# Kernel tuning notes

Measured on AMD Instinct MI355X. Metric: run time of the kernel, lower is better.

## Reference

```python
import jax, jax.numpy as jnp
import numpy as np

B, N, XDIM, EDIM, H = 4, 256, 256, 128, 8
DF = XDIM // H


def _linear_params(key, din, dout):
    k1, k2 = jax.random.split(key)
    s = 1.0 / np.sqrt(din)
    W = jax.random.uniform(k1, (din, dout), minval=-s, maxval=s, dtype=jnp.float32)
    b = jax.random.uniform(k2, (dout,), minval=-s, maxval=s, dtype=jnp.float32)
    return W, b


def setup_inputs() -> dict:
    key = jax.random.key(0)
    ks = jax.random.split(key, 9)
    x = jax.random.normal(ks[0], (B, N, XDIM), dtype=jnp.float32)
    e = jax.random.normal(ks[1], (B, N, N, EDIM), dtype=jnp.float32)
    Wq, bq = _linear_params(ks[2], XDIM, XDIM)
    Wk, bk = _linear_params(ks[3], XDIM, XDIM)
    Wv, bv = _linear_params(ks[4], XDIM, XDIM)
    Wem, bem = _linear_params(ks[5], EDIM, XDIM)  # e_mul
    Wea, bea = _linear_params(ks[6], EDIM, XDIM)  # e_add
    Wxo, bxo = _linear_params(ks[7], XDIM, XDIM)  # x_out
    Weo, beo = _linear_params(ks[8], XDIM, EDIM)  # e_out
    return {"x": x, "e": e, "Wq": Wq, "bq": bq, "Wk": Wk, "bk": bk,
            "Wv": Wv, "bv": bv, "Wem": Wem, "bem": bem, "Wea": Wea, "bea": bea,
            "Wxo": Wxo, "bxo": bxo, "Weo": Weo, "beo": beo}


def reference(x, e, Wq, bq, Wk, bk, Wv, bv, Wem, bem, Wea, bea, Wxo, bxo, Weo, beo):
    Bq, Nq, _ = x.shape
    # per-node projections -> [B, N, H, DF]
    Q = (x @ Wq + bq).reshape(Bq, Nq, H, DF)
    K = (x @ Wk + bk).reshape(Bq, Nq, H, DF)
    V = (x @ Wv + bv).reshape(Bq, Nq, H, DF)
    # broadcasted outer product: Y[b,i,j,h,d] = Q[b,i,h,d] * K[b,j,h,d] / sqrt(DF)
    Y = Q[:, :, None] * K[:, None] * (1.0 / np.sqrt(DF))  # [B,N,N,H,DF]
    # edge modulation
    E1 = (e @ Wem + bem).reshape(Bq, Nq, Nq, H, DF)
    E2 = (e @ Wea + bea).reshape(Bq, Nq, Nq, H, DF)
    Y = Y * (E1 + 1.0) + E2
    # new edge features
    newE = Y.reshape(Bq, Nq, Nq, XDIM) @ Weo + beo  # [B,N,N,EDIM]
    # attention: softmax over the FIRST node axis (dim=1), as in the torch code
    attn = jax.nn.softmax(Y, axis=1)  # [B,N,N,H,DF]
    # weighted_V[b,j,h,d] = sum_i attn[b,i,j,h,d] * V[b,j,h,d]
    weighted_V = jnp.sum(attn * V[:, None], axis=1)  # [B,N,H,DF]
    newX = weighted_V.reshape(Bq, Nq, XDIM) @ Wxo + bxo  # [B,N,XDIM]
    return (newX, newE)
```

## Files before the change

kernel.cpp:

```cpp
#include <hip/hip_runtime.h>

#define NN 256
#define XD 256
#define ED 128

typedef __attribute__((ext_vector_type(8))) short short8;
typedef __attribute__((ext_vector_type(4))) float f32x4;
typedef __attribute__((ext_vector_type(2))) unsigned int uint2v;

__device__ __forceinline__ unsigned short f2bf(float f) {
    unsigned u = __builtin_bit_cast(unsigned, f);
    u += 0x7FFF + ((u >> 16) & 1);
    return (unsigned short)(u >> 16);
}

__device__ __forceinline__ unsigned cvtpk(float lo, float hi) {
    unsigned r;
    asm("v_cvt_pk_bf16_f32 %0, %1, %2" : "=v"(r) : "v"(lo), "v"(hi));
    return r;
}

#define MFMA16(a, b, c) __builtin_amdgcn_mfma_f32_16x16x32_bf16(a, b, c, 0, 0, 0)

__global__ __launch_bounds__(256) void wprep_kernel(
    const float* __restrict__ Wq, const float* __restrict__ Wk,
    const float* __restrict__ Wv, const float* __restrict__ Wxo,
    const float* __restrict__ Wem, const float* __restrict__ Wea,
    const float* __restrict__ Weo,
    short* __restrict__ WqT, short* __restrict__ WkT,
    short* __restrict__ WvT, short* __restrict__ WxoT,
    short* __restrict__ WemT, short* __restrict__ WeaT,
    short* __restrict__ WeoT)
{
    __shared__ float sT[32][33];
    int blk = blockIdx.x;
    const float* src; short* dst; int din, dout, tile;
    if (blk < 256) {
        int m = blk >> 6; tile = blk & 63; din = 256; dout = 256;
        src = m == 0 ? Wq : (m == 1 ? Wk : (m == 2 ? Wv : Wxo));
        dst = m == 0 ? WqT : (m == 1 ? WkT : (m == 2 ? WvT : WxoT));
    } else if (blk < 320) {
        int m = (blk - 256) >> 5; tile = (blk - 256) & 31; din = 128; dout = 256;
        src = m == 0 ? Wem : Wea; dst = m == 0 ? WemT : WeaT;
    } else {
        tile = blk - 320; din = 256; dout = 128;
        src = Weo; dst = WeoT;
    }
    int ksh = (din == 256) ? 3 : 2;
    int kt = tile & ((1 << ksh) - 1);
    int nt = tile >> ksh;
    int c = threadIdx.x & 31, rbase = threadIdx.x >> 5;
    #pragma unroll
    for (int p = 0; p < 4; ++p) {
        int r = rbase + p * 8;
        sT[r][c] = src[(kt * 32 + r) * dout + nt * 32 + c];
    }
    __syncthreads();
    #pragma unroll
    for (int p = 0; p < 4; ++p) {
        int r = rbase + p * 8;
        dst[(nt * 32 + r) * din + kt * 32 + c] = (short)f2bf(sT[c][r]);
    }
}

__global__ __launch_bounds__(512) void proj_all_kernel(
    const float* __restrict__ x,
    const short* __restrict__ WqT, const short* __restrict__ WkT,
    const short* __restrict__ WvT, const short* __restrict__ WxoT,
    const float* __restrict__ bq, const float* __restrict__ bk,
    const float* __restrict__ bv, const float* __restrict__ bxo,
    float* __restrict__ Qs, float* __restrict__ Ks, float* __restrict__ outX)
{
    __shared__ unsigned short sX[64 * 264];
    __shared__ unsigned short sV[64 * 264];
    const int blk = blockIdx.x;
    const bool isvx = blk >= 32;
    const int mtile = isvx ? (blk - 32) : (blk >> 1);
    const int tid = threadIdx.x, wave = tid >> 6, lane = tid & 63;
    const int quad = lane >> 4, l16 = lane & 15;

    {
        const float4* src4 = (const float4*)(x + (size_t)mtile * 64 * XD);
        #pragma unroll
        for (int it = 0; it < 8; ++it) {
            int idx4 = tid + it * 512;
            float4 v = src4[idx4];
            int elem = idx4 * 4, row = elem >> 8, col = elem & 255;
            uint2v p; p.x = cvtpk(v.x, v.y); p.y = cvtpk(v.z, v.w);
            *(uint2v*)&sX[row * 264 + col] = p;
        }
    }
    __syncthreads();

    const int c0 = wave * 32;

    if (!isvx) {
        const int mat  = blk & 1;
        const short* WT   = mat ? WkT : WqT;
        const float* bias = mat ? bk : bq;
        const float scale = mat ? 1.0f : 0.17677669529663687f;
        float* out        = mat ? Ks : Qs;
        f32x4 acc[4][2] = {};
        for (int ks = 0; ks < 8; ++ks) {
            short8 bfrag[2];
            #pragma unroll
            for (int ct = 0; ct < 2; ++ct)
                bfrag[ct] = *(const short8*)&WT[(c0 + ct * 16 + l16) * 256 + ks * 32 + quad * 8];
            #pragma unroll
            for (int mt = 0; mt < 4; ++mt) {
                short8 a = *(const short8*)&sX[(mt * 16 + l16) * 264 + ks * 32 + quad * 8];
                acc[mt][0] = MFMA16(a, bfrag[0], acc[mt][0]);
                acc[mt][1] = MFMA16(a, bfrag[1], acc[mt][1]);
            }
        }
        #pragma unroll
        for (int mt = 0; mt < 4; ++mt)
            #pragma unroll
            for (int ct = 0; ct < 2; ++ct) {
                int cc = c0 + ct * 16 + l16;
                float bb = bias[cc];
                #pragma unroll
                for (int r = 0; r < 4; ++r)
                    out[(size_t)(mtile * 64 + mt * 16 + quad * 4 + r) * 256 + cc] =
                        (acc[mt][ct][r] + bb) * scale;
            }
    } else {
        f32x4 acc[4][2] = {};
        for (int ks = 0; ks < 8; ++ks) {
            short8 bfrag[2];
            #pragma unroll
            for (int ct = 0; ct < 2; ++ct)
                bfrag[ct] = *(const short8*)&WvT[(c0 + ct * 16 + l16) * 256 + ks * 32 + quad * 8];
            #pragma unroll
            for (int mt = 0; mt < 4; ++mt) {
                short8 a = *(const short8*)&sX[(mt * 16 + l16) * 264 + ks * 32 + quad * 8];
                acc[mt][0] = MFMA16(a, bfrag[0], acc[mt][0]);
                acc[mt][1] = MFMA16(a, bfrag[1], acc[mt][1]);
            }
        }
        #pragma unroll
        for (int mt = 0; mt < 4; ++mt)
            #pragma unroll
            for (int ct = 0; ct < 2; ++ct) {
                int cc = c0 + ct * 16 + l16;
                float bb = bv[cc];
                #pragma unroll
                for (int r = 0; r < 4; ++r)
                    sV[(mt * 16 + quad * 4 + r) * 264 + cc] = f2bf(acc[mt][ct][r] + bb);
            }
        __syncthreads();
        f32x4 acc2[4][2] = {};
        for (int ks = 0; ks < 8; ++ks) {
            short8 bfrag[2];
            #pragma unroll
            for (int ct = 0; ct < 2; ++ct)
                bfrag[ct] = *(const short8*)&WxoT[(c0 + ct * 16 + l16) * 256 + ks * 32 + quad * 8];
            #pragma unroll
            for (int mt = 0; mt < 4; ++mt) {
                short8 a = *(const short8*)&sV[(mt * 16 + l16) * 264 + ks * 32 + quad * 8];
                acc2[mt][0] = MFMA16(a, bfrag[0], acc2[mt][0]);
                acc2[mt][1] = MFMA16(a, bfrag[1], acc2[mt][1]);
            }
        }
        #pragma unroll
        for (int mt = 0; mt < 4; ++mt)
            #pragma unroll
            for (int ct = 0; ct < 2; ++ct) {
                int cc = c0 + ct * 16 + l16;
                float bb = bxo[cc];
                #pragma unroll
                for (int r = 0; r < 4; ++r)
                    outX[(size_t)(mtile * 64 + mt * 16 + quad * 4 + r) * 256 + cc] =
                        acc2[mt][ct][r] + bb;
            }
    }
}

__global__ __launch_bounds__(256, 3) void fused_edge_kernel(
    const float* __restrict__ e, const float* __restrict__ Qs,
    const float* __restrict__ Ks, const short* __restrict__ WemT,
    const short* __restrict__ WeaT, const short* __restrict__ WeoT,
    const float* __restrict__ bem, const float* __restrict__ bea,
    const float* __restrict__ beo, float* __restrict__ outE)
{
    __shared__ unsigned short sE[64 * 140];
    __shared__ unsigned short sY[64 * 268];

    const int blk  = blockIdx.x;
    const int jq   = blk & 3;
    const int i    = (blk >> 2) & 255;
    const int b    = blk >> 10;
    const int j0   = jq * 64;
    const int tid  = threadIdx.x;
    const int wave = tid >> 6;
    const int lane = tid & 63;
    const int quad = lane >> 4;
    const int l16  = lane & 15;

    {
        const float4* src4 = (const float4*)(e + (size_t)((b * NN + i) * NN + j0) * ED);
        float4 ev[8];
        #pragma unroll
        for (int it = 0; it < 8; ++it) ev[it] = src4[tid + it * 256];
        #pragma unroll
        for (int it = 0; it < 8; ++it) {
            int idx4 = tid + it * 256;
            int row = idx4 >> 5, col = (idx4 & 31) * 4;
            uint2v p; p.x = cvtpk(ev[it].x, ev[it].y); p.y = cvtpk(ev[it].z, ev[it].w);
            *(uint2v*)&sE[row * 140 + col] = p;
        }
    }
    __syncthreads();

    const int cW = wave * 64;
    const float* Qrow = Qs + (size_t)(b * NN + i) * XD;

    short8 ef[4][4];
    #pragma unroll
    for (int jT = 0; jT < 4; ++jT)
        #pragma unroll
        for (int ks = 0; ks < 4; ++ks)
            ef[jT][ks] = *(const short8*)&sE[(jT * 16 + l16) * 140 + ks * 32 + quad * 8];

    #pragma unroll
    for (int cT = 0; cT < 4; ++cT) {
        const int c0 = cW + cT * 16;
        const int cq = c0 + quad * 4;
        f32x4 q4  = *(const f32x4*)&Qrow[cq];
        f32x4 bm4 = *(const f32x4*)&bem[cq] + 1.0f;
        f32x4 ba4 = *(const f32x4*)&bea[cq];
        f32x4 k4[4];
        #pragma unroll
        for (int jT = 0; jT < 4; ++jT)
            k4[jT] = *(const f32x4*)&Ks[(size_t)(b * NN + j0 + jT * 16 + l16) * XD + cq];

        f32x4 a1[4] = {}, a2[4] = {};
        #pragma unroll
        for (int ks = 0; ks < 4; ++ks) {
            short8 wa = *(const short8*)&WemT[(c0 + l16) * 128 + ks * 32 + quad * 8];
            short8 wb = *(const short8*)&WeaT[(c0 + l16) * 128 + ks * 32 + quad * 8];
            #pragma unroll
            for (int jT = 0; jT < 4; ++jT) {
                a1[jT] = MFMA16(wa, ef[jT][ks], a1[jT]);
                a2[jT] = MFMA16(wb, ef[jT][ks], a2[jT]);
            }
        }
        #pragma unroll
        for (int jT = 0; jT < 4; ++jT) {
            f32x4 y = q4 * k4[jT] * (a1[jT] + bm4) + (a2[jT] + ba4);
            uint2v p; p.x = cvtpk(y[0], y[1]); p.y = cvtpk(y[2], y[3]);
            *(uint2v*)&sY[(jT * 16 + l16) * 268 + cq] = p;
        }
    }

    const int oW = wave * 32;
    short8 wo[4][2];
    #pragma unroll
    for (int ks = 0; ks < 4; ++ks)
        #pragma unroll
        for (int oT = 0; oT < 2; ++oT)
            wo[ks][oT] = *(const short8*)&WeoT[(oW + oT * 16 + l16) * 256 + ks * 32 + quad * 8];
    __syncthreads();

    f32x4 acc[2][4] = {};
    #pragma unroll
    for (int ks = 0; ks < 8; ++ks) {
        short8 w0, w1;
        if (ks < 4) { w0 = wo[ks][0]; w1 = wo[ks][1]; }
        else {
            w0 = *(const short8*)&WeoT[(oW + l16) * 256 + ks * 32 + quad * 8];
            w1 = *(const short8*)&WeoT[(oW + 16 + l16) * 256 + ks * 32 + quad * 8];
        }
        #pragma unroll
        for (int jT = 0; jT < 4; ++jT) {
            short8 yb = *(const short8*)&sY[(jT * 16 + l16) * 268 + ks * 32 + quad * 8];
            acc[0][jT] = MFMA16(w0, yb, acc[0][jT]);
            acc[1][jT] = MFMA16(w1, yb, acc[1][jT]);
        }
    }

    float* outBase = outE + (size_t)((b * NN + i) * NN + j0) * ED;
    #pragma unroll
    for (int oT = 0; oT < 2; ++oT) {
        const int oq = oW + oT * 16 + quad * 4;
        f32x4 bo4 = *(const f32x4*)&beo[oq];
        #pragma unroll
        for (int jT = 0; jT < 4; ++jT) {
            f32x4 st = acc[oT][jT] + bo4;
            *(f32x4*)&outBase[(size_t)(j0 * 0 + jT * 16 + l16) * ED + oq] = st;
        }
    }
}

extern "C" void kernel_launch(void* const* d_in, const int* in_sizes, int n_in,
                              void* d_out, int out_size, void* d_ws, size_t ws_size,
                              hipStream_t stream)
{
    const float* x   = (const float*)d_in[0];
    const float* e   = (const float*)d_in[1];
    const float* Wq  = (const float*)d_in[2];
    const float* bq  = (const float*)d_in[3];
    const float* Wk  = (const float*)d_in[4];
    const float* bk  = (const float*)d_in[5];
    const float* Wv  = (const float*)d_in[6];
    const float* bv  = (const float*)d_in[7];
    const float* Wem = (const float*)d_in[8];
    const float* bem = (const float*)d_in[9];
    const float* Wea = (const float*)d_in[10];
    const float* bea = (const float*)d_in[11];
    const float* Wxo = (const float*)d_in[12];
    const float* bxo = (const float*)d_in[13];
    const float* Weo = (const float*)d_in[14];
    const float* beo = (const float*)d_in[15];

    float* outX = (float*)d_out;
    float* outE = (float*)d_out + 262144;

    float* Qs   = (float*)d_ws;
    float* Ks   = Qs + 262144;
    short* WqT  = (short*)(Ks + 262144);
    short* WkT  = WqT + 65536;
    short* WvT  = WkT + 65536;
    short* WxoT = WvT + 65536;
    short* WemT = WxoT + 65536;
    short* WeaT = WemT + 32768;
    short* WeoT = WeaT + 32768;

    hipLaunchKernelGGL(wprep_kernel, dim3(352), dim3(256), 0, stream,
                       Wq, Wk, Wv, Wxo, Wem, Wea, Weo,
                       WqT, WkT, WvT, WxoT, WemT, WeaT, WeoT);
    hipLaunchKernelGGL(proj_all_kernel, dim3(48), dim3(512), 0, stream,
                       x, WqT, WkT, WvT, WxoT, bq, bk, bv, bxo, Qs, Ks, outX);
    hipLaunchKernelGGL(fused_edge_kernel, dim3(4096), dim3(256), 0, stream,
                       e, Qs, Ks, WemT, WeaT, WeoT, bem, bea, beo, outE);
}
```

Before: 381.4 us.

## Loop each edge block over four j-tiles with register-prefetched next e tile

The edge kernel now launches one block per (b,i) row and loops over the four 64-column j tiles, instead of one block per tile. While the Weo GEMM runs, the next e tile is loaded into registers and written to shared memory afterwards, so global latency overlaps with MFMA work. The output GEMM is also remapped so each wave covers 64 output columns × 2 j-tiles, which changes how Weo fragments and Y are reused. The cost is a quarter as many blocks (1024 on a large GPU), more live registers, and extra barriers per iteration.

```diff
diff --git a/kernel.cpp b/kernel.cpp
--- a/kernel.cpp
+++ b/kernel.cpp
@@ -187,21 +187,20 @@
     __shared__ unsigned short sY[64 * 268];
 
     const int blk  = blockIdx.x;
-    const int jq   = blk & 3;
-    const int i    = (blk >> 2) & 255;
-    const int b    = blk >> 10;
-    const int j0   = jq * 64;
+    const int i    = blk & 255;
+    const int b    = blk >> 8;
     const int tid  = threadIdx.x;
     const int wave = tid >> 6;
     const int lane = tid & 63;
     const int quad = lane >> 4;
     const int l16  = lane & 15;
 
+    const float4* ebase = (const float4*)(e + (size_t)((b * NN + i) * NN) * ED);
+
     {
-        const float4* src4 = (const float4*)(e + (size_t)((b * NN + i) * NN + j0) * ED);
         float4 ev[8];
         #pragma unroll
-        for (int it = 0; it < 8; ++it) ev[it] = src4[tid + it * 256];
+        for (int it = 0; it < 8; ++it) ev[it] = ebase[tid + it * 256];
         #pragma unroll
         for (int it = 0; it < 8; ++it) {
             int idx4 = tid + it * 256;
@@ -212,83 +211,99 @@
     }
     __syncthreads();
 
+    const float* Qrow = Qs + (size_t)(b * NN + i) * XD;
     const int cW = wave * 64;
-    const float* Qrow = Qs + (size_t)(b * NN + i) * XD;
-
-    short8 ef[4][4];
-    #pragma unroll
-    for (int jT = 0; jT < 4; ++jT)
-        #pragma unroll
-        for (int ks = 0; ks < 4; ++ks)
-            ef[jT][ks] = *(const short8*)&sE[(jT * 16 + l16) * 140 + ks * 32 + quad * 8];
-
-    #pragma unroll
-    for (int cT = 0; cT < 4; ++cT) {
-        const int c0 = cW + cT * 16;
-        const int cq = c0 + quad * 4;
-        f32x4 q4  = *(const f32x4*)&Qrow[cq];
-        f32x4 bm4 = *(const f32x4*)&bem[cq] + 1.0f;
-        f32x4 ba4 = *(const f32x4*)&bea[cq];
-        f32x4 k4[4];
+    const int oH = (wave & 1) * 64;
+    const int jH = (wave >> 1) * 2;
+
+    #pragma unroll 1
+    for (int t = 0; t < 4; ++t) {
+        const int j0 = t * 64;
+
+        short8 efr[4][4];
         #pragma unroll
         for (int jT = 0; jT < 4; ++jT)
-            k4[jT] = *(const f32x4*)&Ks[(size_t)(b * NN + j0 + jT * 16 + l16) * XD + cq];
-
-        f32x4 a1[4] = {}, a2[4] = {};
-        #pragma unroll
-        for (int ks = 0; ks < 4; ++ks) {
-            short8 wa = *(const short8*)&WemT[(c0 + l16) * 128 + ks * 32 + quad * 8];
-            short8 wb = *(const short8*)&WeaT[(c0 + l16) * 128 + ks * 32 + quad * 8];
+            #pragma unroll
+            for (int ks = 0; ks < 4; ++ks)
+                efr[jT][ks] = *(const short8*)&sE[(jT * 16 + l16) * 140 + ks * 32 + quad * 8];
+
+        #pragma unroll
+        for (int cT = 0; cT < 4; ++cT) {
+            const int c0 = cW + cT * 16;
+            const int cq = c0 + quad * 4;
+            f32x4 q4  = *(const f32x4*)&Qrow[cq];
+            f32x4 bm4 = *(const f32x4*)&bem[cq] + 1.0f;
+            f32x4 ba4 = *(const f32x4*)&bea[cq];
+            f32x4 k4[4];
+            #pragma unroll
+            for (int jT = 0; jT < 4; ++jT)
+                k4[jT] = *(const f32x4*)&Ks[(size_t)(b * NN + j0 + jT * 16 + l16) * XD + cq];
+
+            f32x4 a1[4] = {}, a2[4] = {};
+            #pragma unroll
+            for (int ks = 0; ks < 4; ++ks) {
+                short8 wa = *(const short8*)&WemT[(c0 + l16) * 128 + ks * 32 + quad * 8];
+                short8 wb = *(const short8*)&WeaT[(c0 + l16) * 128 + ks * 32 + quad * 8];
+                #pragma unroll
+                for (int jT = 0; jT < 4; ++jT) {
+                    a1[jT] = MFMA16(wa, efr[jT][ks], a1[jT]);
+                    a2[jT] = MFMA16(wb, efr[jT][ks], a2[jT]);
+                }
+            }
             #pragma unroll
             for (int jT = 0; jT < 4; ++jT) {
-                a1[jT] = MFMA16(wa, ef[jT][ks], a1[jT]);
-                a2[jT] = MFMA16(wb, ef[jT][ks], a2[jT]);
-            }
-        }
-        #pragma unroll
-        for (int jT = 0; jT < 4; ++jT) {
-            f32x4 y = q4 * k4[jT] * (a1[jT] + bm4) + (a2[jT] + ba4);
-            uint2v p; p.x = cvtpk(y[0], y[1]); p.y = cvtpk(y[2], y[3]);
-            *(uint2v*)&sY[(jT * 16 + l16) * 268 + cq] = p;
-        }
-    }
-
-    const int oW = wave * 32;
-    short8 wo[4][2];
-    #pragma unroll
-    for (int ks = 0; ks < 4; ++ks)
-        #pragma unroll
-        for (int oT = 0; oT < 2; ++oT)
-            wo[ks][oT] = *(const short8*)&WeoT[(oW + oT * 16 + l16) * 256 + ks * 32 + quad * 8];
-    __syncthreads();
-
-    f32x4 acc[2][4] = {};
-    #pragma unroll
-    for (int ks = 0; ks < 8; ++ks) {
-        short8 w0, w1;
-        if (ks < 4) { w0 = wo[ks][0]; w1 = wo[ks][1]; }
-        else {
-            w0 = *(const short8*)&WeoT[(oW + l16) * 256 + ks * 32 + quad * 8];
-            w1 = *(const short8*)&WeoT[(oW + 16 + l16) * 256 + ks * 32 + quad * 8];
-        }
-        #pragma unroll
-        for (int jT = 0; jT < 4; ++jT) {
-            short8 yb = *(const short8*)&sY[(jT * 16 + l16) * 268 + ks * 32 + quad * 8];
-            acc[0][jT] = MFMA16(w0, yb, acc[0][jT]);
-            acc[1][jT] = MFMA16(w1, yb, acc[1][jT]);
-        }
-    }
-
-    float* outBase = outE + (size_t)((b * NN + i) * NN + j0) * ED;
-    #pragma unroll
-    for (int oT = 0; oT < 2; ++oT) {
-        const int oq = oW + oT * 16 + quad * 4;
-        f32x4 bo4 = *(const f32x4*)&beo[oq];
-        #pragma unroll
-        for (int jT = 0; jT < 4; ++jT) {
-            f32x4 st = acc[oT][jT] + bo4;
-            *(f32x4*)&outBase[(size_t)(j0 * 0 + jT * 16 + l16) * ED + oq] = st;
-        }
+                f32x4 y = q4 * k4[jT] * (a1[jT] + bm4) + (a2[jT] + ba4);
+                uint2v p; p.x = cvtpk(y[0], y[1]); p.y = cvtpk(y[2], y[3]);
+                *(uint2v*)&sY[(jT * 16 + l16) * 268 + cq] = p;
+            }
+        }
+        __syncthreads();
+
+        float4 ev[8];
+        if (t < 3) {
+            #pragma unroll
+            for (int it = 0; it < 8; ++it)
+                ev[it] = ebase[(t + 1) * 2048 + tid + it * 256];
+        }
+
+        f32x4 acc[4][2] = {};
+        #pragma unroll
+        for (int ks = 0; ks < 8; ++ks) {
+            short8 wo[4];
+            #pragma unroll
+            for (int oT = 0; oT < 4; ++oT)
+                wo[oT] = *(const short8*)&WeoT[(oH + oT * 16 + l16) * 256 + ks * 32 + quad * 8];
+            #pragma unroll
+            for (int jt = 0; jt < 2; ++jt) {
+                short8 yb = *(const short8*)&sY[((jH + jt) * 16 + l16) * 268 + ks * 32 + quad * 8];
+                #pragma unroll
+                for (int oT = 0; oT < 4; ++oT)
+                    acc[oT][jt] = MFMA16(wo[oT], yb, acc[oT][jt]);
+            }
+        }
+
+        if (t < 3) {
+            #pragma unroll
+            for (int it = 0; it < 8; ++it) {
+                int idx4 = tid + it * 256;
+                int row = idx4 >> 5, col = (idx4 & 31) * 4;
+                uint2v p; p.x = cvtpk(ev[it].x, ev[it].y); p.y = cvtpk(ev[it].z, ev[it].w);
+                *(uint2v*)&sE[row * 140 + col] = p;
+            }
+        }
+
+        float* outBase = outE + (size_t)((b * NN + i) * NN + j0) * ED;
+        #pragma unroll
+        for (int oT = 0; oT < 4; ++oT) {
+            const int oq = oH + oT * 16 + quad * 4;
+            f32x4 bo4 = *(const f32x4*)&beo[oq];
+            #pragma unroll
+            for (int jt = 0; jt < 2; ++jt) {
+                f32x4 st = acc[oT][jt] + bo4;
+                *(f32x4*)&outBase[(size_t)((jH + jt) * 16 + l16) * ED + oq] = st;
+            }
+        }
+        __syncthreads();
     }
 }
 
@@ -331,6 +346,6 @@
                        WqT, WkT, WvT, WxoT, WemT, WeaT, WeoT);
     hipLaunchKernelGGL(proj_all_kernel, dim3(48), dim3(512), 0, stream,
                        x, WqT, WkT, WvT, WxoT, bq, bk, bv, bxo, Qs, Ks, outX);
-    hipLaunchKernelGGL(fused_edge_kernel, dim3(4096), dim3(256), 0, stream,
+    hipLaunchKernelGGL(fused_edge_kernel, dim3(1024), dim3(256), 0, stream,
                        e, Qs, Ks, WemT, WeaT, WeoT, bem, bea, beo, outE);
 }
```

After: 553.0 us. +45.0%, slower.

## Split edge kernel Y computation into two halves to shrink LDS and raise occupancy

Applied to the files above, without the earlier changes.

The fused edge kernel now computes the 256-wide Y tile in two 128-column passes, each followed by its half of the e_out GEMM reduction. This halves the sY shared buffer, and the e fragments are re-read from LDS instead of being held in registers, so launch bounds can request 4 blocks per SM instead of 3. The cost is extra barriers, repeated LDS reads of the e tile, and weight fragments that are no longer preloaded.

```diff
diff --git a/kernel.cpp b/kernel.cpp
--- a/kernel.cpp
+++ b/kernel.cpp
@@ -176,7 +176,7 @@
     }
 }
 
-__global__ __launch_bounds__(256, 3) void fused_edge_kernel(
+__global__ __launch_bounds__(256, 4) void fused_edge_kernel(
     const float* __restrict__ e, const float* __restrict__ Qs,
     const float* __restrict__ Ks, const short* __restrict__ WemT,
     const short* __restrict__ WeaT, const short* __restrict__ WeoT,
@@ -184,7 +184,7 @@
     const float* __restrict__ beo, float* __restrict__ outE)
 {
     __shared__ unsigned short sE[64 * 140];
-    __shared__ unsigned short sY[64 * 268];
+    __shared__ unsigned short sY[64 * 140];
 
     const int blk  = blockIdx.x;
     const int jq   = blk & 3;
@@ -212,71 +212,58 @@
     }
     __syncthreads();
 
-    const int cW = wave * 64;
     const float* Qrow = Qs + (size_t)(b * NN + i) * XD;
-
-    short8 ef[4][4];
+    const int oW = wave * 32;
+    f32x4 acc[2][4] = {};
+
     #pragma unroll
-    for (int jT = 0; jT < 4; ++jT)
-        #pragma unroll
-        for (int ks = 0; ks < 4; ++ks)
-            ef[jT][ks] = *(const short8*)&sE[(jT * 16 + l16) * 140 + ks * 32 + quad * 8];
-
-    #pragma unroll
-    for (int cT = 0; cT < 4; ++cT) {
-        const int c0 = cW + cT * 16;
-        const int cq = c0 + quad * 4;
-        f32x4 q4  = *(const f32x4*)&Qrow[cq];
-        f32x4 bm4 = *(const f32x4*)&bem[cq] + 1.0f;
-        f32x4 ba4 = *(const f32x4*)&bea[cq];
-        f32x4 k4[4];
-        #pragma unroll
-        for (int jT = 0; jT < 4; ++jT)
-            k4[jT] = *(const f32x4*)&Ks[(size_t)(b * NN + j0 + jT * 16 + l16) * XD + cq];
-
-        f32x4 a1[4] = {}, a2[4] = {};
+    for (int p = 0; p < 2; ++p) {
+        #pragma unroll
+        for (int cT = 0; cT < 2; ++cT) {
+            const int cl = wave * 32 + cT * 16;
+            const int c0 = p * 128 + cl;
+            const int cq = c0 + quad * 4;
+            f32x4 q4  = *(const f32x4*)&Qrow[cq];
+            f32x4 bm4 = *(const f32x4*)&bem[cq] + 1.0f;
+            f32x4 ba4 = *(const f32x4*)&bea[cq];
+            f32x4 k4[4];
+            #pragma unroll
+            for (int jT = 0; jT < 4; ++jT)
+                k4[jT] = *(const f32x4*)&Ks[(size_t)(b * NN + j0 + jT * 16 + l16) * XD + cq];
+
+            f32x4 a1[4] = {}, a2[4] = {};
+            #pragma unroll
+            for (int ks = 0; ks < 4; ++ks) {
+                short8 wa = *(const short8*)&WemT[(c0 + l16) * 128 + ks * 32 + quad * 8];
+                short8 wb = *(const short8*)&WeaT[(c0 + l16) * 128 + ks * 32 + quad * 8];
+                #pragma unroll
+                for (int jT = 0; jT < 4; ++jT) {
+                    short8 ef = *(const short8*)&sE[(jT * 16 + l16) * 140 + ks * 32 + quad * 8];
+                    a1[jT] = MFMA16(wa, ef, a1[jT]);
+                    a2[jT] = MFMA16(wb, ef, a2[jT]);
+                }
+            }
+            #pragma unroll
+            for (int jT = 0; jT < 4; ++jT) {
+                f32x4 y = q4 * k4[jT] * (a1[jT] + bm4) + (a2[jT] + ba4);
+                uint2v pk; pk.x = cvtpk(y[0], y[1]); pk.y = cvtpk(y[2], y[3]);
+                *(uint2v*)&sY[(jT * 16 + l16) * 140 + cl + quad * 4] = pk;
+            }
+        }
+        __syncthreads();
+
         #pragma unroll
         for (int ks = 0; ks < 4; ++ks) {
-            short8 wa = *(const short8*)&WemT[(c0 + l16) * 128 + ks * 32 + quad * 8];
-            short8 wb = *(const short8*)&WeaT[(c0 + l16) * 128 + ks * 32 + quad * 8];
+            short8 w0 = *(const short8*)&WeoT[(oW + l16) * 256 + (p * 4 + ks) * 32 + quad * 8];
+            short8 w1 = *(const short8*)&WeoT[(oW + 16 + l16) * 256 + (p * 4 + ks) * 32 + quad * 8];
             #pragma unroll
             for (int jT = 0; jT < 4; ++jT) {
-                a1[jT] = MFMA16(wa, ef[jT][ks], a1[jT]);
-                a2[jT] = MFMA16(wb, ef[jT][ks], a2[jT]);
-            }
-        }
-        #pragma unroll
-        for (int jT = 0; jT < 4; ++jT) {
-            f32x4 y = q4 * k4[jT] * (a1[jT] + bm4) + (a2[jT] + ba4);
-            uint2v p; p.x = cvtpk(y[0], y[1]); p.y = cvtpk(y[2], y[3]);
-            *(uint2v*)&sY[(jT * 16 + l16) * 268 + cq] = p;
-        }
-    }
-
-    const int oW = wave * 32;
-    short8 wo[4][2];
-    #pragma unroll
-    for (int ks = 0; ks < 4; ++ks)
-        #pragma unroll
-        for (int oT = 0; oT < 2; ++oT)
-            wo[ks][oT] = *(const short8*)&WeoT[(oW + oT * 16 + l16) * 256 + ks * 32 + quad * 8];
-    __syncthreads();
-
-    f32x4 acc[2][4] = {};
-    #pragma unroll
-    for (int ks = 0; ks < 8; ++ks) {
-        short8 w0, w1;
-        if (ks < 4) { w0 = wo[ks][0]; w1 = wo[ks][1]; }
-        else {
-            w0 = *(const short8*)&WeoT[(oW + l16) * 256 + ks * 32 + quad * 8];
-            w1 = *(const short8*)&WeoT[(oW + 16 + l16) * 256 + ks * 32 + quad * 8];
-        }
-        #pragma unroll
-        for (int jT = 0; jT < 4; ++jT) {
-            short8 yb = *(const short8*)&sY[(jT * 16 + l16) * 268 + ks * 32 + quad * 8];
-            acc[0][jT] = MFMA16(w0, yb, acc[0][jT]);
-            acc[1][jT] = MFMA16(w1, yb, acc[1][jT]);
-        }
+                short8 yb = *(const short8*)&sY[(jT * 16 + l16) * 140 + ks * 32 + quad * 8];
+                acc[0][jT] = MFMA16(w0, yb, acc[0][jT]);
+                acc[1][jT] = MFMA16(w1, yb, acc[1][jT]);
+            }
+        }
+        if (p == 0) __syncthreads();
     }
 
     float* outBase = outE + (size_t)((b * NN + i) * NN + j0) * ED;
@@ -287,7 +274,7 @@
         #pragma unroll
         for (int jT = 0; jT < 4; ++jT) {
             f32x4 st = acc[oT][jT] + bo4;
-            *(f32x4*)&outBase[(size_t)(j0 * 0 + jT * 16 + l16) * ED + oq] = st;
+            *(f32x4*)&outBase[(size_t)(jT * 16 + l16) * ED + oq] = st;
         }
     }
 }
```

Result: slower. 399.0 us (+4.6%).
